# Kernel tuning notes

Measured on AMD Instinct MI355X. Metric: run time of the kernel, lower is better.

The kernel has to match this reference:

```python
import jax, jax.numpy as jnp
import numpy as np

B, N, C, H = 16, 640, 640, 8      # frames, tokens/frame (20*32 latent), channels, heads
D = C // H                        # 80 head dim
N_SEL = 2048                      # number of SACFA-masked tokens gathered across all frames


def setup_inputs() -> dict:
    key = jax.random.key(0)
    ks = jax.random.split(key, 7)
    x = jax.random.normal(ks[0], (B, N, C), jnp.float32)
    s = C ** -0.5
    Wq = jax.random.normal(ks[1], (C, C), jnp.float32) * s
    Wk = jax.random.normal(ks[2], (C, C), jnp.float32) * s
    Wv = jax.random.normal(ks[3], (C, C), jnp.float32) * s
    Wo = jax.random.normal(ks[4], (C, C), jnp.float32) * s
    bo = jnp.zeros((C,), jnp.float32)
    # binary SACFA mask over flattened (B*N) tokens with exactly N_SEL ones
    perm = jax.random.permutation(ks[5], B * N)
    sacfa_mask = jnp.zeros((B * N,), jnp.float32).at[perm[:N_SEL]].set(1.0)
    return {"x": x, "Wq": Wq, "Wk": Wk, "Wv": Wv, "Wo": Wo, "bo": bo,
            "sacfa_mask": sacfa_mask, "n_sel": N_SEL}


def reference(x, Wq, Wk, Wv, Wo, bo, sacfa_mask, n_sel):
    b, n, c = x.shape
    h = H
    d = c // h
    # QKV projections (self-attention: context = x)
    q = x @ Wq
    k = x @ Wk
    v = x @ Wv
    # SACFA: gather boolean-masked tokens from all frames (static count n_sel)
    sel = jnp.nonzero(sacfa_mask > 0.5, size=n_sel)[0]           # [n_sel]
    k_tok = k.reshape(b * n, c)[sel]                              # [n_sel, c]
    v_tok = v.reshape(b * n, c)[sel]
    # repeat shared tokens per frame and concat along kv sequence
    k = jnp.concatenate([k, jnp.broadcast_to(k_tok, (b, n_sel, c))], axis=1)
    v = jnp.concatenate([v, jnp.broadcast_to(v_tok, (b, n_sel, c))], axis=1)
    # head split: b s (h d) -> b h s d
    to_heads = lambda t: t.reshape(b, -1, h, d).transpose(0, 2, 1, 3)
    qh, kh, vh = to_heads(q), to_heads(k), to_heads(v)
    # scaled dot-product attention (math of xformers memory_efficient_attention)
    scores = jnp.einsum('bhqd,bhkd->bhqk', qh, kh) * (d ** -0.5)  # [b,h,n,n+n_sel]
    attn = jax.nn.softmax(scores, axis=-1)
    out = jnp.einsum('bhqk,bhkd->bhqd', attn, vh)
    out = out.transpose(0, 2, 1, 3).reshape(b, n, c)              # b h n d -> b n c
    return out @ Wo + bo
```

## Files before the change

### kernel.cpp

```cpp
#include <hip/hip_runtime.h>
#include <hip/hip_bf16.h>

#define B_    16
#define N_    640
#define C_    640
#define H_    8
#define D_    80
#define DP_   96
#define CP_   768
#define NSEL_ 2048
#define NTOK_ 10240
#define NKV_  12288

typedef short bf16x8 __attribute__((ext_vector_type(8)));
typedef float f32x4  __attribute__((ext_vector_type(4)));
typedef unsigned int u32;
typedef u32 u32x4 __attribute__((ext_vector_type(4)));
typedef unsigned short u16;

#define MFMA16(a,b,c) __builtin_amdgcn_mfma_f32_16x16x32_bf16((a),(b),(c),0,0,0)

static __device__ __forceinline__ u16 f2b(float f) {
  u32 x = __builtin_bit_cast(u32, f);
  x += 0x7fffu + ((x >> 16) & 1u);
  return (u16)(x >> 16);
}

static __device__ __forceinline__ u32 cvtpk(float lo, float hi) {
  u32 r;
  asm("v_cvt_pk_bf16_f32 %0, %1, %2" : "=v"(r) : "v"(lo), "v"(hi));
  return r;
}

static __device__ __forceinline__ void gl16(const void* g, void* l) {
  __builtin_amdgcn_global_load_lds((const __attribute__((address_space(1))) u32*)g,
                                   (__attribute__((address_space(3))) u32*)l, 16, 0, 0);
}

static __device__ __forceinline__ int PI(int r) {
  return ((r >> 2) & 3) * 8 + (r >> 5) * 32 + ((r >> 4) & 1) * 4 + (r & 3);
}

__global__ __launch_bounds__(256) void k_convert_x(const float* __restrict__ x,
                                                   u16* __restrict__ xb) {
  int i = blockIdx.x * 256 + threadIdx.x;
  float4 v = ((const float4*)x)[i];
  ushort4 o;
  o.x = f2b(v.x); o.y = f2b(v.y); o.z = f2b(v.z); o.w = f2b(v.w);
  ((ushort4*)xb)[i] = o;
}

__global__ __launch_bounds__(256) void k_convert_w(const float* w0, const float* w1,
                                                   const float* w2, const float* w3,
                                                   u16* t0, u16* t1, u16* t2, u16* t3) {
  const float* W = (blockIdx.z == 0) ? w0 : (blockIdx.z == 1) ? w1 : (blockIdx.z == 2) ? w2 : w3;
  u16*         T = (blockIdx.z == 0) ? t0 : (blockIdx.z == 1) ? t1 : (blockIdx.z == 2) ? t2 : t3;
  __shared__ float tile[32][33];
  int tx = threadIdx.x & 31, ty = threadIdx.x >> 5;
  int n0 = blockIdx.x * 32, k0 = blockIdx.y * 32;
#pragma unroll
  for (int r = 0; r < 4; r++)
    tile[ty + 8 * r][tx] = W[(k0 + ty + 8 * r) * C_ + n0 + tx];
  __syncthreads();
#pragma unroll
  for (int r = 0; r < 4; r++)
    T[(n0 + ty + 8 * r) * C_ + k0 + tx] = f2b(tile[tx][ty + 8 * r]);
}

__global__ __launch_bounds__(1024) void k_scan(const float* __restrict__ mask,
                                               int* __restrict__ sel) {
  __shared__ int wcnt[16];
  __shared__ int carry;
  int tid = threadIdx.x, lane = tid & 63, wid = tid >> 6;
  float v[10];
#pragma unroll
  for (int r = 0; r < 10; r++) v[r] = mask[r * 1024 + tid];
  if (tid == 0) carry = 0;
  __syncthreads();
  for (int r = 0; r < 10; r++) {
    bool p = v[r] > 0.5f;
    unsigned long long b = __ballot(p);
    if (lane == 0) wcnt[wid] = __popcll(b);
    __syncthreads();
    int off = carry;
    for (int w = 0; w < wid; w++) off += wcnt[w];
    if (p) sel[off + __popcll(b & ((1ull << lane) - 1ull))] = r * 1024 + tid;
    __syncthreads();
    if (tid == 0) {
      int s = 0;
      for (int w = 0; w < 16; w++) s += wcnt[w];
      carry += s;
    }
    __syncthreads();
  }
}

#define QSCALE_ (1.4426950408889634f * 0.11180339887498949f)

template <int MODE>
__global__ __launch_bounds__(256) void k_gemm(const u16* __restrict__ A,
                                              const u16* __restrict__ BT,
                                              void* __restrict__ out,
                                              const float* __restrict__ bias) {
  __shared__ u16 lA[128 * 32];
  __shared__ u16 lB[128 * 32];
  int tid = threadIdx.x, lane = tid & 63, wid = tid >> 6;
  int l15 = lane & 15, l4 = lane >> 4;
  int f = blockIdx.x;
  int m0 = (f % 80) * 128, n0 = (f / 80) * 128;
  int wr = wid >> 1, wc = wid & 1;
  int tok = tid >> 2, ch = tid & 3;
  int sc = ch ^ (tok & 3);
  f32x4 acc[4][4];
#pragma unroll
  for (int mi = 0; mi < 4; mi++)
#pragma unroll
    for (int ni = 0; ni < 4; ni++) acc[mi][ni] = (f32x4){0.f, 0.f, 0.f, 0.f};

  for (int k0 = 0; k0 < C_; k0 += 32) {
    __syncthreads();
    gl16(A  + (m0 + tok)      * C_ + k0 + sc * 8, (char*)lA + tid * 16);
    gl16(A  + (m0 + tok + 64) * C_ + k0 + sc * 8, (char*)lA + 4096 + tid * 16);
    gl16(BT + (n0 + tok)      * C_ + k0 + sc * 8, (char*)lB + tid * 16);
    gl16(BT + (n0 + tok + 64) * C_ + k0 + sc * 8, (char*)lB + 4096 + tid * 16);
    __syncthreads();
    bf16x8 af[4], bfr[4];
#pragma unroll
    for (int mi = 0; mi < 4; mi++) {
      int r = wr * 64 + mi * 16 + l15;
      af[mi] = *(const bf16x8*)((const char*)lA + r * 64 + ((l4 ^ (r & 3)) * 16));
    }
#pragma unroll
    for (int ni = 0; ni < 4; ni++) {
      int r = wc * 64 + ni * 16 + l15;
      bfr[ni] = *(const bf16x8*)((const char*)lB + r * 64 + ((l4 ^ (r & 3)) * 16));
    }
#pragma unroll
    for (int mi = 0; mi < 4; mi++)
#pragma unroll
      for (int ni = 0; ni < 4; ni++) acc[mi][ni] = MFMA16(af[mi], bfr[ni], acc[mi][ni]);
  }

  int cbase = n0 + wc * 64, rbase = m0 + wr * 64;
  if (MODE == 0 || MODE == 1) {
    u16* P = (u16*)out;
#pragma unroll
    for (int mi = 0; mi < 4; mi++)
#pragma unroll
      for (int ni = 0; ni < 4; ni++) {
        int c = cbase + ni * 16 + l15;
        int h = c / 80, d = c % 80;
#pragma unroll
        for (int rg = 0; rg < 4; rg++) {
          int r = rbase + mi * 16 + l4 * 4 + rg;
          float v = acc[mi][ni][rg];
          if (MODE == 0) v *= QSCALE_;
          P[r * CP_ + h * DP_ + d] = f2b(v);
        }
      }
  } else if (MODE == 2) {
    u16* P = (u16*)out;
#pragma unroll
    for (int mi = 0; mi < 4; mi++)
#pragma unroll
      for (int ni = 0; ni < 4; ni++) {
        int c = cbase + ni * 16 + l15;
        int r0 = rbase + mi * 16 + l4 * 4;
        ushort4 pk;
        pk.x = f2b(acc[mi][ni][0]); pk.y = f2b(acc[mi][ni][1]);
        pk.z = f2b(acc[mi][ni][2]); pk.w = f2b(acc[mi][ni][3]);
        *(ushort4*)(P + c * NKV_ + r0) = pk;
      }
  } else {
    float* P = (float*)out;
#pragma unroll
    for (int ni = 0; ni < 4; ni++) {
      int c = cbase + ni * 16 + l15;
      float bv = bias[c];
#pragma unroll
      for (int mi = 0; mi < 4; mi++)
#pragma unroll
        for (int rg = 0; rg < 4; rg++)
          P[(rbase + mi * 16 + l4 * 4 + rg) * C_ + c] = acc[mi][ni][rg] + bv;
    }
  }
}

__global__ __launch_bounds__(256) void k_gather(const int* __restrict__ sel,
                                                u16* __restrict__ Kp,
                                                u16* __restrict__ Vt) {
  int i = blockIdx.x;
  int t = threadIdx.x;
  int s = sel[i];
  const u32* src = (const u32*)(Kp + s * CP_);
  u32* dst = (u32*)(Kp + (NTOK_ + i) * CP_);
  dst[t] = src[t];
  if (t < 128) dst[256 + t] = src[256 + t];
  for (int c = t; c < C_; c += 256)
    Vt[c * NKV_ + NTOK_ + i] = Vt[c * NKV_ + s];
}

__global__ __launch_bounds__(256, 2) void k_attn(const u16* __restrict__ Qp,
                                                 const u16* __restrict__ Kp,
                                                 const u16* __restrict__ Vt,
                                                 u16* __restrict__ Ob) {
  __shared__ u16 smem[2][10240];
  int tid = threadIdx.x, lane = tid & 63, wid = tid >> 6;
  int l15 = lane & 15, l4 = lane >> 4;
  int f = blockIdx.x;
  int b = f & 15, h = (f >> 4) & 7, qt = f >> 7;
  int q0 = qt * 128 + wid * 32;
  const int NT = 42;
  const bf16x8 kz = {0, 0, 0, 0, 0, 0, 0, 0};

  bf16x8 qf[2][2], qtl[2];
#pragma unroll
  for (int m = 0; m < 2; m++) {
    const u16* qrow = Qp + (size_t)(b * N_ + q0 + m * 16 + l15) * CP_ + h * DP_;
#pragma unroll
    for (int kk = 0; kk < 2; kk++)
      qf[m][kk] = *(const bf16x8*)(qrow + kk * 32 + l4 * 8);
    qtl[m] = (l4 < 2) ? *(const bf16x8*)(qrow + 64 + l4 * 8) : kz;
  }

  f32x4 o[2][5];
#pragma unroll
  for (int m = 0; m < 2; m++)
#pragma unroll
    for (int d5 = 0; d5 < 5; d5++) o[m][d5] = (f32x4){0.f, 0.f, 0.f, 0.f};
  float li_[2] = {0.f, 0.f};

  u32 gof[5];
#pragma unroll
  for (int k = 0; k < 5; k++) {
    int s = tid + 256 * k;
    if (s < 512) {
      int kk = s >> 8, rem = s & 255, tok = rem >> 2, c = rem & 3;
      gof[k] = (u32)(PI(tok) * CP_ + h * DP_ + kk * 32 + ((c ^ (tok & 3)) * 8));
    } else if (s < 640) {
      int j = s - 512, tok = j >> 1, ch = j & 1;
      gof[k] = (u32)(PI(tok) * CP_ + h * DP_ + 64 + ch * 8);
    } else {
      int j = s - 640, vd = j >> 3, c = j & 7;
      gof[k] = (u32)((h * D_ + vd) * NKV_ + ((c ^ (vd & 7)) * 8));
    }
  }

  auto stage = [&](int g, int buf) {
    int tokbase = (g < 10) ? (b * N_ + g * 64) : (NTOK_ + (g - 10) * 64);
    size_t kadd = (size_t)tokbase * CP_;
    char* dst = (char*)smem[buf] + tid * 16;
#pragma unroll
    for (int k = 0; k < 5; k++) {
      bool isv = (k >= 3) || (k == 2 && tid >= 128);
      const u16* src = isv ? (Vt + gof[k] + tokbase) : (Kp + gof[k] + kadd);
      gl16(src, dst + k * 4096);
    }
  };

  stage(0, 0);
  __syncthreads();
  int cur = 0;

  for (int tt = 0; tt < NT; tt++) {
    if (tt + 1 < NT) stage(tt + 1, cur ^ 1);
    const char* kb0 = (const char*)smem[cur];
    const char* vb0 = kb0 + 10240;

    bf16x8 kb[12];
#pragma unroll
    for (int kk = 0; kk < 2; kk++)
#pragma unroll
      for (int nt = 0; nt < 4; nt++) {
        int tk = nt * 16 + l15;
        kb[kk * 4 + nt] = *(const bf16x8*)(kb0 + kk * 4096 + tk * 64 + ((l4 ^ (tk & 3)) * 16));
      }
#pragma unroll
    for (int nt = 0; nt < 4; nt++) {
      int tk = nt * 16 + l15;
      bf16x8 t = *(const bf16x8*)(kb0 + 8192 + tk * 32 + ((l4 & 1) * 16));
      kb[8 + nt] = (l4 < 2) ? t : kz;
    }
    bf16x8 vb[10];
#pragma unroll
    for (int kk2 = 0; kk2 < 2; kk2++)
#pragma unroll
      for (int d5 = 0; d5 < 5; d5++) {
        int dd = d5 * 16 + l15;
        vb[kk2 * 5 + d5] =
            *(const bf16x8*)(vb0 + dd * 128 + (((kk2 * 4 + l4) ^ (dd & 7)) * 16));
      }

    f32x4 s[2][4];
#pragma unroll
    for (int m = 0; m < 2; m++)
#pragma unroll
      for (int nt = 0; nt < 4; nt++) s[m][nt] = (f32x4){0.f, 0.f, 0.f, 0.f};
    __builtin_amdgcn_s_setprio(1);
#pragma unroll
    for (int kk = 0; kk < 2; kk++)
#pragma unroll
      for (int nt = 0; nt < 4; nt++) {
        s[0][nt] = MFMA16(kb[kk * 4 + nt], qf[0][kk], s[0][nt]);
        s[1][nt] = MFMA16(kb[kk * 4 + nt], qf[1][kk], s[1][nt]);
      }
#pragma unroll
    for (int nt = 0; nt < 4; nt++) {
      s[0][nt] = MFMA16(kb[8 + nt], qtl[0], s[0][nt]);
      s[1][nt] = MFMA16(kb[8 + nt], qtl[1], s[1][nt]);
    }
    __builtin_amdgcn_s_setprio(0);

#pragma unroll
    for (int m = 0; m < 2; m++) {
#pragma unroll
      for (int nt = 0; nt < 4; nt++)
#pragma unroll
        for (int rg = 0; rg < 4; rg++)
          s[m][nt][rg] = exp2f(s[m][nt][rg]);
      f32x4 ps = (s[m][0] + s[m][1]) + (s[m][2] + s[m][3]);
      li_[m] += (ps[0] + ps[1]) + (ps[2] + ps[3]);
    }

    bf16x8 pa[2][2];
#pragma unroll
    for (int m = 0; m < 2; m++)
#pragma unroll
      for (int kk2 = 0; kk2 < 2; kk2++) {
        u32x4 w;
        w.x = cvtpk(s[m][2 * kk2][0],     s[m][2 * kk2][1]);
        w.y = cvtpk(s[m][2 * kk2][2],     s[m][2 * kk2][3]);
        w.z = cvtpk(s[m][2 * kk2 + 1][0], s[m][2 * kk2 + 1][1]);
        w.w = cvtpk(s[m][2 * kk2 + 1][2], s[m][2 * kk2 + 1][3]);
        pa[m][kk2] = __builtin_bit_cast(bf16x8, w);
      }

    __builtin_amdgcn_s_setprio(1);
#pragma unroll
    for (int kk2 = 0; kk2 < 2; kk2++)
#pragma unroll
      for (int d5 = 0; d5 < 5; d5++) {
        o[0][d5] = MFMA16(pa[0][kk2], vb[kk2 * 5 + d5], o[0][d5]);
        o[1][d5] = MFMA16(pa[1][kk2], vb[kk2 * 5 + d5], o[1][d5]);
      }
    __builtin_amdgcn_s_setprio(0);

    __syncthreads();
    cur ^= 1;
  }

#pragma unroll
  for (int m = 0; m < 2; m++) {
    li_[m] += __shfl_xor(li_[m], 16);
    li_[m] += __shfl_xor(li_[m], 32);
  }
#pragma unroll
  for (int m = 0; m < 2; m++)
#pragma unroll
    for (int rg = 0; rg < 4; rg++) {
      float lv = __shfl(li_[m], l4 * 4 + rg);
      float inv = 1.f / lv;
#pragma unroll
      for (int d5 = 0; d5 < 5; d5++) {
        int r = b * N_ + q0 + m * 16 + l4 * 4 + rg;
        Ob[(size_t)r * C_ + h * D_ + d5 * 16 + l15] = f2b(o[m][d5][rg] * inv);
      }
    }
}

extern "C" void kernel_launch(void* const* d_in, const int* in_sizes, int n_in,
                              void* d_out, int out_size, void* d_ws, size_t ws_size,
                              hipStream_t stream) {
  (void)in_sizes; (void)n_in; (void)out_size; (void)ws_size;
  const float* x    = (const float*)d_in[0];
  const float* Wq   = (const float*)d_in[1];
  const float* Wk   = (const float*)d_in[2];
  const float* Wv   = (const float*)d_in[3];
  const float* Wo   = (const float*)d_in[4];
  const float* bo   = (const float*)d_in[5];
  const float* mask = (const float*)d_in[6];

  char* ws = (char*)d_ws;
  u16* xb  = (u16*)(ws + 0);
  u16* Ob  = xb;
  u16* WqT = (u16*)(ws + 13107200);
  u16* WkT = (u16*)(ws + 13926400);
  u16* WvT = (u16*)(ws + 14745600);
  u16* WoT = (u16*)(ws + 15564800);
  u16* Qp  = (u16*)(ws + 16384000);
  u16* Kp  = (u16*)(ws + 32112640);
  u16* Vt  = (u16*)(ws + 50987008);
  int* sel = (int*)(ws + 66715648);

  k_convert_x<<<6400, 256, 0, stream>>>(x, xb);
  k_convert_w<<<dim3(20, 20, 4), 256, 0, stream>>>(Wq, Wk, Wv, Wo, WqT, WkT, WvT, WoT);
  k_scan<<<1, 1024, 0, stream>>>(mask, sel);
  k_gemm<1><<<400, 256, 0, stream>>>(xb, WkT, Kp, nullptr);
  k_gemm<2><<<400, 256, 0, stream>>>(xb, WvT, Vt, nullptr);
  k_gather<<<2048, 256, 0, stream>>>(sel, Kp, Vt);
  k_gemm<0><<<400, 256, 0, stream>>>(xb, WqT, Qp, nullptr);
  k_attn<<<640, 256, 0, stream>>>(Qp, Kp, Vt, Ob);
  k_gemm<3><<<400, 256, 0, stream>>>(Ob, WoT, d_out, bo);
}
```

Before: 236.9 us.

## Merge QKV GEMMs into one launch; load V fragments directly from global in attention

The three Q/K/V projection GEMMs are combined into a single 1200-block launch that picks its weight matrix and epilogue from the block index. This removes two launch gaps and gives the GPU more concurrent blocks. In the attention kernel, V tiles are no longer staged through LDS. Each lane now reads its bf16x8 V fragments straight from global memory, which halves the shared-memory footprint and the staging traffic. In exchange, the V loads are issued synchronously at the top of each iteration, so global latency may be exposed to the MFMA work unless caching and the extra occupancy hide it.

```diff
diff --git a/kernel.cpp b/kernel.cpp
--- a/kernel.cpp
+++ b/kernel.cpp
@@ -97,11 +97,89 @@
 
 #define QSCALE_ (1.4426950408889634f * 0.11180339887498949f)
 
-template <int MODE>
-__global__ __launch_bounds__(256) void k_gemm(const u16* __restrict__ A,
-                                              const u16* __restrict__ BT,
-                                              void* __restrict__ out,
-                                              const float* __restrict__ bias) {
+__global__ __launch_bounds__(256) void k_gemm_qkv(const u16* __restrict__ A,
+                                                  const u16* __restrict__ WkT,
+                                                  const u16* __restrict__ WvT,
+                                                  const u16* __restrict__ WqT,
+                                                  u16* __restrict__ Kp,
+                                                  u16* __restrict__ Vt,
+                                                  u16* __restrict__ Qp) {
+  __shared__ u16 lA[128 * 32];
+  __shared__ u16 lB[128 * 32];
+  int tid = threadIdx.x, lane = tid & 63, wid = tid >> 6;
+  int l15 = lane & 15, l4 = lane >> 4;
+  int f = blockIdx.x;
+  int which = f / 400, g = f % 400;
+  const u16* BT = (which == 0) ? WkT : (which == 1) ? WvT : WqT;
+  int m0 = (g % 80) * 128, n0 = (g / 80) * 128;
+  int wr = wid >> 1, wc = wid & 1;
+  int tok = tid >> 2, ch = tid & 3;
+  int sc = ch ^ (tok & 3);
+  f32x4 acc[4][4];
+#pragma unroll
+  for (int mi = 0; mi < 4; mi++)
+#pragma unroll
+    for (int ni = 0; ni < 4; ni++) acc[mi][ni] = (f32x4){0.f, 0.f, 0.f, 0.f};
+
+  for (int k0 = 0; k0 < C_; k0 += 32) {
+    __syncthreads();
+    gl16(A  + (m0 + tok)      * C_ + k0 + sc * 8, (char*)lA + tid * 16);
+    gl16(A  + (m0 + tok + 64) * C_ + k0 + sc * 8, (char*)lA + 4096 + tid * 16);
+    gl16(BT + (n0 + tok)      * C_ + k0 + sc * 8, (char*)lB + tid * 16);
+    gl16(BT + (n0 + tok + 64) * C_ + k0 + sc * 8, (char*)lB + 4096 + tid * 16);
+    __syncthreads();
+    bf16x8 af[4], bfr[4];
+#pragma unroll
+    for (int mi = 0; mi < 4; mi++) {
+      int r = wr * 64 + mi * 16 + l15;
+      af[mi] = *(const bf16x8*)((const char*)lA + r * 64 + ((l4 ^ (r & 3)) * 16));
+    }
+#pragma unroll
+    for (int ni = 0; ni < 4; ni++) {
+      int r = wc * 64 + ni * 16 + l15;
+      bfr[ni] = *(const bf16x8*)((const char*)lB + r * 64 + ((l4 ^ (r & 3)) * 16));
+    }
+#pragma unroll
+    for (int mi = 0; mi < 4; mi++)
+#pragma unroll
+      for (int ni = 0; ni < 4; ni++) acc[mi][ni] = MFMA16(af[mi], bfr[ni], acc[mi][ni]);
+  }
+
+  int cbase = n0 + wc * 64, rbase = m0 + wr * 64;
+  if (which == 1) {
+#pragma unroll
+    for (int mi = 0; mi < 4; mi++)
+#pragma unroll
+      for (int ni = 0; ni < 4; ni++) {
+        int c = cbase + ni * 16 + l15;
+        int r0 = rbase + mi * 16 + l4 * 4;
+        ushort4 pk;
+        pk.x = f2b(acc[mi][ni][0]); pk.y = f2b(acc[mi][ni][1]);
+        pk.z = f2b(acc[mi][ni][2]); pk.w = f2b(acc[mi][ni][3]);
+        *(ushort4*)(Vt + c * NKV_ + r0) = pk;
+      }
+  } else {
+    u16* P = (which == 0) ? Kp : Qp;
+    float sc2 = (which == 2) ? QSCALE_ : 1.f;
+#pragma unroll
+    for (int mi = 0; mi < 4; mi++)
+#pragma unroll
+      for (int ni = 0; ni < 4; ni++) {
+        int c = cbase + ni * 16 + l15;
+        int h = c / 80, d = c % 80;
+#pragma unroll
+        for (int rg = 0; rg < 4; rg++) {
+          int r = rbase + mi * 16 + l4 * 4 + rg;
+          P[r * CP_ + h * DP_ + d] = f2b(acc[mi][ni][rg] * sc2);
+        }
+      }
+  }
+}
+
+__global__ __launch_bounds__(256) void k_gemm_o(const u16* __restrict__ A,
+                                                const u16* __restrict__ BT,
+                                                float* __restrict__ out,
+                                                const float* __restrict__ bias) {
   __shared__ u16 lA[128 * 32];
   __shared__ u16 lB[128 * 32];
   int tid = threadIdx.x, lane = tid & 63, wid = tid >> 6;
@@ -142,47 +220,15 @@
   }
 
   int cbase = n0 + wc * 64, rbase = m0 + wr * 64;
-  if (MODE == 0 || MODE == 1) {
-    u16* P = (u16*)out;
+#pragma unroll
+  for (int ni = 0; ni < 4; ni++) {
+    int c = cbase + ni * 16 + l15;
+    float bv = bias[c];
 #pragma unroll
     for (int mi = 0; mi < 4; mi++)
 #pragma unroll
-      for (int ni = 0; ni < 4; ni++) {
-        int c = cbase + ni * 16 + l15;
-        int h = c / 80, d = c % 80;
-#pragma unroll
-        for (int rg = 0; rg < 4; rg++) {
-          int r = rbase + mi * 16 + l4 * 4 + rg;
-          float v = acc[mi][ni][rg];
-          if (MODE == 0) v *= QSCALE_;
-          P[r * CP_ + h * DP_ + d] = f2b(v);
-        }
-      }
-  } else if (MODE == 2) {
-    u16* P = (u16*)out;
-#pragma unroll
-    for (int mi = 0; mi < 4; mi++)
-#pragma unroll
-      for (int ni = 0; ni < 4; ni++) {
-        int c = cbase + ni * 16 + l15;
-        int r0 = rbase + mi * 16 + l4 * 4;
-        ushort4 pk;
-        pk.x = f2b(acc[mi][ni][0]); pk.y = f2b(acc[mi][ni][1]);
-        pk.z = f2b(acc[mi][ni][2]); pk.w = f2b(acc[mi][ni][3]);
-        *(ushort4*)(P + c * NKV_ + r0) = pk;
-      }
-  } else {
-    float* P = (float*)out;
-#pragma unroll
-    for (int ni = 0; ni < 4; ni++) {
-      int c = cbase + ni * 16 + l15;
-      float bv = bias[c];
-#pragma unroll
-      for (int mi = 0; mi < 4; mi++)
-#pragma unroll
-        for (int rg = 0; rg < 4; rg++)
-          P[(rbase + mi * 16 + l4 * 4 + rg) * C_ + c] = acc[mi][ni][rg] + bv;
-    }
+      for (int rg = 0; rg < 4; rg++)
+        out[(rbase + mi * 16 + l4 * 4 + rg) * C_ + c] = acc[mi][ni][rg] + bv;
   }
 }
 
@@ -204,7 +250,7 @@
                                                  const u16* __restrict__ Kp,
                                                  const u16* __restrict__ Vt,
                                                  u16* __restrict__ Ob) {
-  __shared__ u16 smem[2][10240];
+  __shared__ u16 smem[2][5120];
   int tid = threadIdx.x, lane = tid & 63, wid = tid >> 6;
   int l15 = lane & 15, l4 = lane >> 4;
   int f = blockIdx.x;
@@ -230,9 +276,9 @@
     for (int d5 = 0; d5 < 5; d5++) o[m][d5] = (f32x4){0.f, 0.f, 0.f, 0.f};
   float li_[2] = {0.f, 0.f};
 
-  u32 gof[5];
-#pragma unroll
-  for (int k = 0; k < 5; k++) {
+  u32 gof[3];
+#pragma unroll
+  for (int k = 0; k < 3; k++) {
     int s = tid + 256 * k;
     if (s < 512) {
       int kk = s >> 8, rem = s & 255, tok = rem >> 2, c = rem & 3;
@@ -241,8 +287,7 @@
       int j = s - 512, tok = j >> 1, ch = j & 1;
       gof[k] = (u32)(PI(tok) * CP_ + h * DP_ + 64 + ch * 8);
     } else {
-      int j = s - 640, vd = j >> 3, c = j & 7;
-      gof[k] = (u32)((h * D_ + vd) * NKV_ + ((c ^ (vd & 7)) * 8));
+      gof[k] = 0;
     }
   }
 
@@ -250,22 +295,30 @@
     int tokbase = (g < 10) ? (b * N_ + g * 64) : (NTOK_ + (g - 10) * 64);
     size_t kadd = (size_t)tokbase * CP_;
     char* dst = (char*)smem[buf] + tid * 16;
-#pragma unroll
-    for (int k = 0; k < 5; k++) {
-      bool isv = (k >= 3) || (k == 2 && tid >= 128);
-      const u16* src = isv ? (Vt + gof[k] + tokbase) : (Kp + gof[k] + kadd);
-      gl16(src, dst + k * 4096);
-    }
+    gl16(Kp + gof[0] + kadd, dst);
+    gl16(Kp + gof[1] + kadd, dst + 4096);
+    if (tid < 128) gl16(Kp + gof[2] + kadd, dst + 8192);
   };
+
+  const u16* vbase = Vt + (size_t)(h * D_ + l15) * NKV_ + l4 * 8;
 
   stage(0, 0);
   __syncthreads();
   int cur = 0;
 
   for (int tt = 0; tt < NT; tt++) {
+    int tokbase = (tt < 10) ? (b * N_ + tt * 64) : (NTOK_ + (tt - 10) * 64);
+
+    bf16x8 vb[10];
+#pragma unroll
+    for (int kk2 = 0; kk2 < 2; kk2++)
+#pragma unroll
+      for (int d5 = 0; d5 < 5; d5++)
+        vb[kk2 * 5 + d5] =
+            *(const bf16x8*)(vbase + (size_t)d5 * 16 * NKV_ + kk2 * 32 + tokbase);
+
     if (tt + 1 < NT) stage(tt + 1, cur ^ 1);
     const char* kb0 = (const char*)smem[cur];
-    const char* vb0 = kb0 + 10240;
 
     bf16x8 kb[12];
 #pragma unroll
@@ -281,15 +334,6 @@
       bf16x8 t = *(const bf16x8*)(kb0 + 8192 + tk * 32 + ((l4 & 1) * 16));
       kb[8 + nt] = (l4 < 2) ? t : kz;
     }
-    bf16x8 vb[10];
-#pragma unroll
-    for (int kk2 = 0; kk2 < 2; kk2++)
-#pragma unroll
-      for (int d5 = 0; d5 < 5; d5++) {
-        int dd = d5 * 16 + l15;
-        vb[kk2 * 5 + d5] =
-            *(const bf16x8*)(vb0 + dd * 128 + (((kk2 * 4 + l4) ^ (dd & 7)) * 16));
-      }
 
     f32x4 s[2][4];
 #pragma unroll
@@ -395,10 +439,8 @@
   k_convert_x<<<6400, 256, 0, stream>>>(x, xb);
   k_convert_w<<<dim3(20, 20, 4), 256, 0, stream>>>(Wq, Wk, Wv, Wo, WqT, WkT, WvT, WoT);
   k_scan<<<1, 1024, 0, stream>>>(mask, sel);
-  k_gemm<1><<<400, 256, 0, stream>>>(xb, WkT, Kp, nullptr);
-  k_gemm<2><<<400, 256, 0, stream>>>(xb, WvT, Vt, nullptr);
+  k_gemm_qkv<<<1200, 256, 0, stream>>>(xb, WkT, WvT, WqT, Kp, Vt, Qp);
   k_gather<<<2048, 256, 0, stream>>>(sel, Kp, Vt);
-  k_gemm<0><<<400, 256, 0, stream>>>(xb, WqT, Qp, nullptr);
   k_attn<<<640, 256, 0, stream>>>(Qp, Kp, Vt, Ob);
-  k_gemm<3><<<400, 256, 0, stream>>>(Ob, WoT, d_out, bo);
-}
+  k_gemm_o<<<400, 256, 0, stream>>>(Ob, WoT, (float*)d_out, bo);
+}
```

New measurement: 291.8 us. 23.2% more time.
